# Optimization experiments

Measured on AMD Instinct MI355X. Metric: run time of the kernel, lower is better.

The kernel has to match this reference:

```python
import jax, jax.numpy as jnp
import numpy as np

EPS = 1e-8
LRELU_SLOPE = 0.2


def leaky_relu(x, p=LRELU_SLOPE):
    return jnp.where(x >= 0, x, p * x)


def conv2dmod(x, weight, style):
    """StyleGAN2 weight-demodulated conv.
    x: [B,C_in,H,W], weight: [C_out,C_in,k,k], style: [B,C_in]."""
    # per-sample modulation: scale input channels by (style + 1)
    w = weight[None] * (style[:, None, :, None, None] + 1.0)  # [B,O,I,k,k]
    # demodulation: rescale each output filter to unit norm
    d = jax.lax.rsqrt(jnp.sum(w * w, axis=(2, 3, 4), keepdims=True) + EPS)
    w = w * d

    def conv_one(xi, wi):
        # xi: [C_in,H,W], wi: [O,I,k,k] -> [O,H,W]
        return jax.lax.conv_general_dilated(
            xi[None], wi, window_strides=(1, 1), padding='SAME',
            dimension_numbers=('NCHW', 'OIHW', 'NCHW'))[0]

    return jax.vmap(conv_one)(x, w)  # [B,O,H,W]


def setup_inputs() -> dict:
    key = jax.random.key(0)
    ks = jax.random.split(key, 9)
    B, C_in, C_out, H, W = 16, 128, 256, 128, 128
    return {
        "features": jax.random.normal(ks[0], (B, C_in, H, W), jnp.float32),
        "style_mean1": jax.random.normal(ks[1], (B, C_in, 1, 1), jnp.float32),
        "style_std1": jax.random.normal(ks[2], (B, C_in, 1, 1), jnp.float32),
        "style_mean2": jax.random.normal(ks[3], (B, C_in, 1, 1), jnp.float32),
        "style_std2": jax.random.normal(ks[4], (B, C_in, 1, 1), jnp.float32),
        "lastBlockBool": 0,
        "w1": jax.random.normal(ks[5], (C_in, C_in, 3, 3), jnp.float32),
        "w2": jax.random.normal(ks[6], (C_in, C_in, 3, 3), jnp.float32),
        "down_w": jax.random.normal(ks[7], (C_out, C_in, 4, 4), jnp.float32) * 0.05,
        "down_b": jnp.zeros((C_out,), jnp.float32),
    }


def reference(features, style_mean1, style_std1, style_mean2, style_std2,
              lastBlockBool, w1, w2, down_w, down_b):
    # style_mean2/style_std2/lastBlockBool are accepted but unused by the
    # original forward; dropout is identity (eval mode).
    s1 = style_mean1[:, :, 0, 0]  # squeeze(-1).squeeze(-1) -> [B,C_in]
    s2 = style_std1[:, :, 0, 0]
    x = leaky_relu(conv2dmod(features, w1, s1))
    x = leaky_relu(conv2dmod(x, w2, s2) + x)  # residual
    # downsample: 4x4 conv, stride 2, pad 1 -> halves H,W
    y = jax.lax.conv_general_dilated(
        x, down_w, window_strides=(2, 2), padding=((1, 1), (1, 1)),
        dimension_numbers=('NCHW', 'OIHW', 'NCHW'))
    return y + down_b[None, :, None, None]
```

## Files before the change

kernel.cpp:

```cpp
#include <hip/hip_runtime.h>
#include <hip/hip_bf16.h>

constexpr int B  = 16;
constexpr int C  = 128;
constexpr int H  = 128;
constexpr int W  = 128;
constexpr int CO = 256;
constexpr int HO = 64;
constexpr int WO = 64;

#define EPSV   1e-8f
#define SLOPE  0.2f

typedef short bf16x8 __attribute__((ext_vector_type(8)));
typedef float f32x4  __attribute__((ext_vector_type(4)));

typedef const __attribute__((address_space(1))) unsigned int  gbl_u32;
typedef __attribute__((address_space(3))) unsigned int        lds_u32;

__device__ __forceinline__ void bar_raw() {
    asm volatile("" ::: "memory");
    __builtin_amdgcn_s_barrier();
    asm volatile("" ::: "memory");
}
#define WAITV(N) asm volatile("s_waitcnt vmcnt(" #N ")" ::: "memory")

__device__ __forceinline__ short f2bs(float v) {
    __hip_bfloat16 h = __float2bfloat16(v);
    return *(short*)&h;
}
__device__ __forceinline__ float bs2f(short s) {
    __hip_bfloat16 h = *(__hip_bfloat16*)&s;
    return __bfloat162float(h);
}

__global__ __launch_bounds__(128) void demod_kernel(
    const float* __restrict__ w1, const float* __restrict__ w2,
    const float* __restrict__ s1, const float* __restrict__ s2,
    float* __restrict__ d)
{
    int bid  = blockIdx.x;
    int conv = bid >> 11;
    int b    = (bid >> 7) & 15;
    int o    = bid & 127;
    const float* w = conv ? w2 : w1;
    const float* s = conv ? s2 : s1;
    int i = threadIdx.x;
    float sv = s[b * C + i] + 1.0f;
    const float* wp = w + (o * C + i) * 9;
    float sum = 0.f;
    #pragma unroll
    for (int k = 0; k < 9; ++k) { float t = wp[k] * sv; sum += t * t; }
    #pragma unroll
    for (int off = 32; off; off >>= 1) sum += __shfl_down(sum, off);
    __shared__ float red[2];
    if ((threadIdx.x & 63) == 0) red[threadIdx.x >> 6] = sum;
    __syncthreads();
    if (threadIdx.x == 0) d[bid] = rsqrtf(red[0] + red[1] + EPSV);
}

__global__ __launch_bounds__(256) void expand_kernel(
    const float* __restrict__ w1, const float* __restrict__ w2,
    const float* __restrict__ s1, const float* __restrict__ s2,
    const float* __restrict__ d, short* __restrict__ wm)
{
    int idx = blockIdx.x * 256 + threadIdx.x;
    int ic  = idx & 127;
    int oc  = (idx >> 7) & 127;
    int t   = idx >> 14;
    int tap = t % 9;
    int cb  = t / 9;
    int b   = cb & 15;
    int conv= cb >> 4;
    const float* w = conv ? w2 : w1;
    const float* s = conv ? s2 : s1;
    float v = w[(oc * C + ic) * 9 + tap] * (s[b * C + ic] + 1.0f)
            * d[(conv * B + b) * C + oc];
    int icH = ic >> 6, icL = (ic >> 5) & 1;
    int dst = cb * 147456
            + ((icH * 18 + tap * 2 + icL) * 8 + (oc >> 4)) * 512
            + ((ic >> 3) & 3) * 128 + (oc & 15) * 8 + (ic & 7);
    wm[dst] = f2bs(v);
}

__global__ __launch_bounds__(256) void dwexpand_kernel(
    const float* __restrict__ dw, short* __restrict__ dwm)
{
    int idx = blockIdx.x * 256 + threadIdx.x;
    int ic  = idx & 127;
    int oc  = (idx >> 7) & 255;
    int tap = idx >> 15;
    int dst = ((ic >> 5) * 16 + tap) * 8192 + (oc >> 7) * 4096
            + ((oc >> 4) & 7) * 512
            + ((ic >> 3) & 3) * 128 + (oc & 15) * 8 + (ic & 7);
    dwm[dst] = f2bs(dw[(oc * C + ic) * 16 + tap]);
}

__global__ __launch_bounds__(256) void nchw2nhwc_kernel(
    const float* __restrict__ in, short* __restrict__ out)
{
    __shared__ short s[128 * 136];
    int bid = blockIdx.x;
    int h = bid & 127, b = bid >> 7;
    int tid = threadIdx.x;
    for (int i = tid; i < 128 * 32; i += 256) {
        int w4 = i & 31, ic = i >> 5;
        float4 v = *(const float4*)&in[((b * C + ic) * H + h) * W + w4 * 4];
        s[(w4 * 4 + 0) * 136 + ic] = f2bs(v.x);
        s[(w4 * 4 + 1) * 136 + ic] = f2bs(v.y);
        s[(w4 * 4 + 2) * 136 + ic] = f2bs(v.z);
        s[(w4 * 4 + 3) * 136 + ic] = f2bs(v.w);
    }
    __syncthreads();
    for (int i = tid; i < 128 * 16; i += 256) {
        int icg = i & 15, w = i >> 4;
        *(uint4*)&out[((b * H + h) * W + w) * C + icg * 8] =
            *(uint4*)&s[w * 136 + icg * 8];
    }
}

__global__ __launch_bounds__(256, 4) void conv3x3_mfma(
    const short* __restrict__ in, const short* __restrict__ wmc,
    const short* __restrict__ res, short* __restrict__ out)
{
    __shared__ short sIn[180 * 64];
    __shared__ short sW[2][4096];

    int bid = blockIdx.x;
    int wt = bid & 7, ht = (bid >> 3) & 15, b = bid >> 7;
    int w0 = wt * 16, h0 = ht * 8;
    int tid  = threadIdx.x;
    int lane = tid & 63, wv = tid >> 6;
    int q = lane >> 4, l15 = lane & 15;
    int wr = wv & 1;
    int wc = wv >> 1;

    const short* wb = wmc + b * 147456;

    auto stageIn = [&](int st) {
        for (int i = tid; i < 180 * 8; i += 256) {
            int slot = i & 7, pix = i >> 3;
            int hl = pix / 18, wl = pix - hl * 18;
            int gh = h0 - 1 + hl, gw = w0 - 1 + wl;
            uint4 v = make_uint4(0u, 0u, 0u, 0u);
            if ((unsigned)gh < (unsigned)H && (unsigned)gw < (unsigned)W)
                v = *(const uint4*)&in[((b * H + gh) * W + gw) * C + st * 64 + slot * 8];
            *(uint4*)&sIn[pix * 64 + ((slot ^ (pix & 7)) << 3)] = v;
        }
    };
    auto stageW = [&](int st, int s, int buf) {
        #pragma unroll
        for (int i = 0; i < 2; ++i) {
            const short* g = wb + st * 73728 + s * 4096
                           + (wv * 2 + i) * 512 + lane * 8;
            __builtin_amdgcn_global_load_lds(
                (gbl_u32*)g, (lds_u32*)&sW[buf][(wv * 2 + i) * 512], 16, 0, 0);
        }
    };

    f32x4 acc[4][4];
    #pragma unroll
    for (int mt = 0; mt < 4; ++mt)
        #pragma unroll
        for (int nt = 0; nt < 4; ++nt)
            acc[mt][nt] = (f32x4){0.f, 0.f, 0.f, 0.f};

    stageW(0, 0, 0);
    stageIn(0);
    __syncthreads();

    int bfbase = q * 128 + l15 * 8;

    #pragma unroll 1
    for (int st = 0; st < 2; ++st) {
        #pragma unroll 2
        for (int s = 0; s < 18; ++s) {
            int tap = s >> 1, icL = s & 1;
            int dh = tap / 3, dwd = tap - dh * 3;
            if (s < 17)        stageW(st, s + 1, (s + 1) & 1);
            else if (st == 0)  stageW(1, 0, 0);
            if (st == 1 && s == 17) { WAITV(0); } else { WAITV(2); }
            bar_raw();
            bf16x8 af[4], bf[4];
            #pragma unroll
            for (int mt = 0; mt < 4; ++mt) {
                int pix  = (wr * 4 + mt + dh) * 18 + l15 + dwd;
                int slot = (icL * 4 + q) ^ (pix & 7);
                af[mt] = *(const bf16x8*)&sIn[pix * 64 + slot * 8];
            }
            #pragma unroll
            for (int nt = 0; nt < 4; ++nt)
                bf[nt] = *(const bf16x8*)&sW[s & 1][(wc * 4 + nt) * 512 + bfbase];
            #pragma unroll
            for (int mt = 0; mt < 4; ++mt)
                #pragma unroll
                for (int nt = 0; nt < 4; ++nt)
                    acc[mt][nt] = __builtin_amdgcn_mfma_f32_16x16x32_bf16(
                        af[mt], bf[nt], acc[mt][nt], 0, 0, 0);
            bar_raw();
        }
        if (st == 0) { stageIn(1); __syncthreads(); }
    }

    bool has_res = (res != nullptr);
    #pragma unroll
    for (int mt = 0; mt < 4; ++mt) {
        int h = h0 + wr * 4 + mt;
        #pragma unroll
        for (int nt = 0; nt < 4; ++nt) {
            int oc = wc * 64 + nt * 16 + l15;
            #pragma unroll
            for (int reg = 0; reg < 4; ++reg) {
                int w = w0 + q * 4 + reg;
                int idx = ((b * H + h) * W + w) * C + oc;
                float v = acc[mt][nt][reg];
                if (has_res) v += bs2f(res[idx]);
                v = v >= 0.f ? v : SLOPE * v;
                out[idx] = f2bs(v);
            }
        }
    }
}

__global__ __launch_bounds__(256, 2) void downconv_mfma(
    const short* __restrict__ in, const short* __restrict__ dwm,
    const float* __restrict__ db, float* __restrict__ out)
{
    __shared__ short sIn[2 * 306 * 32];
    __shared__ short sW[2][4096];

    int bid = blockIdx.x;
    int wt = bid & 3;
    int ht = (bid >> 2) & 7;
    int ot = (bid >> 5) & 1;
    int b  = bid >> 6;
    int ow0 = wt * 16, oh0 = ht * 8, oc0 = ot * 128;
    int ih0 = 2 * oh0 - 1, iw0 = 2 * ow0 - 1;

    int tid  = threadIdx.x;
    int lane = tid & 63, wv = tid >> 6;
    int q = lane >> 4, l15 = lane & 15;

    const short* wbase = dwm + ot * 4096;

    auto stageIn = [&](int icC) {
        for (int i = tid; i < 612 * 4; i += 256) {
            int slot = i & 3, pix = i >> 2;
            int ihl = pix / 34, iwl = pix - ihl * 34;
            int gh = ih0 + ihl, gw = iw0 + iwl;
            uint4 v = make_uint4(0u, 0u, 0u, 0u);
            if ((unsigned)gh < (unsigned)H && (unsigned)gw < (unsigned)W)
                v = *(const uint4*)&in[((b * H + gh) * W + gw) * C + icC * 32 + slot * 8];
            int par = iwl & 1, pl = ihl * 17 + (iwl >> 1);
            *(uint4*)&sIn[(par * 306 + pl) * 32 + ((slot ^ ((pl >> 1) & 3)) << 3)] = v;
        }
    };
    auto stageW = [&](int step, int buf) {
        #pragma unroll
        for (int j = 0; j < 2; ++j) {
            int base = (wv * 2 + j) * 512;
            const short* g = wbase + step * 8192 + base + lane * 8;
            __builtin_amdgcn_global_load_lds(
                (gbl_u32*)g, (lds_u32*)&sW[buf][base], 16, 0, 0);
        }
    };

    f32x4 acc[2][8];
    #pragma unroll
    for (int mt = 0; mt < 2; ++mt)
        #pragma unroll
        for (int nt = 0; nt < 8; ++nt)
            acc[mt][nt] = (f32x4){0.f, 0.f, 0.f, 0.f};

    stageW(0, 0);
    stageIn(0);
    __syncthreads();

    int afbase = q * 128 + l15 * 8;

    #pragma unroll 1
    for (int icC = 0; icC < 4; ++icC) {
        #pragma unroll 2
        for (int tap = 0; tap < 16; ++tap) {
            int step = icC * 16 + tap;
            if (step < 63) stageW(step + 1, (step + 1) & 1);
            if (step < 63) { WAITV(2); } else { WAITV(0); }
            bar_raw();
            int dh = tap >> 2, dwn = tap & 3;
            int par = dwn & 1, cb0 = dwn >> 1;
            bf16x8 af[2], bf[8];
            #pragma unroll
            for (int mt = 0; mt < 2; ++mt)
                af[mt] = *(const bf16x8*)&sW[step & 1][(wv * 2 + mt) * 512 + afbase];
            #pragma unroll
            for (int nt = 0; nt < 8; ++nt) {
                int pl = (2 * nt + dh) * 17 + cb0 + l15;
                bf[nt] = *(const bf16x8*)&sIn[(par * 306 + pl) * 32
                                              + ((q ^ ((pl >> 1) & 3)) << 3)];
            }
            #pragma unroll
            for (int mt = 0; mt < 2; ++mt)
                #pragma unroll
                for (int nt = 0; nt < 8; ++nt)
                    acc[mt][nt] = __builtin_amdgcn_mfma_f32_16x16x32_bf16(
                        af[mt], bf[nt], acc[mt][nt], 0, 0, 0);
            bar_raw();
        }
        if (icC < 3) { stageIn(icC + 1); __syncthreads(); }
    }

    #pragma unroll
    for (int mt = 0; mt < 2; ++mt) {
        f32x4 bi = *(const f32x4*)&db[oc0 + (wv * 2 + mt) * 16 + q * 4];
        #pragma unroll
        for (int nt = 0; nt < 8; ++nt) {
            int oh = oh0 + nt;
            #pragma unroll
            for (int reg = 0; reg < 4; ++reg) {
                int oc = oc0 + (wv * 2 + mt) * 16 + q * 4 + reg;
                out[((b * CO + oc) * HO + oh) * WO + ow0 + l15] =
                    acc[mt][nt][reg] + bi[reg];
            }
        }
    }
}

extern "C" void kernel_launch(void* const* d_in, const int* in_sizes, int n_in,
                              void* d_out, int out_size, void* d_ws, size_t ws_size,
                              hipStream_t stream) {
    const float* features = (const float*)d_in[0];
    const float* sm1      = (const float*)d_in[1];
    const float* ss1      = (const float*)d_in[2];
    const float* w1       = (const float*)d_in[6];
    const float* w2       = (const float*)d_in[7];
    const float* dw       = (const float*)d_in[8];
    const float* db       = (const float*)d_in[9];
    float* out = (float*)d_out;

    char* ws = (char*)d_ws;
    short* x1  = (short*)ws;
    short* x2  = (short*)(ws + 67108864);
    short* wm  = (short*)(ws + 134217728);
    short* dwm = (short*)(ws + 143654912);
    float* dv  = (float*)(ws + 144703488);

    demod_kernel    <<<4096, 128, 0, stream>>>(w1, w2, sm1, ss1, dv);
    expand_kernel   <<<18432, 256, 0, stream>>>(w1, w2, sm1, ss1, dv, wm);
    dwexpand_kernel <<<2048, 256, 0, stream>>>(dw, dwm);
    nchw2nhwc_kernel<<<2048, 256, 0, stream>>>(features, x2);
    conv3x3_mfma    <<<2048, 256, 0, stream>>>(x2, wm, nullptr, x1);
    conv3x3_mfma    <<<2048, 256, 0, stream>>>(x1, wm + 16 * 147456, x1, x2);
    downconv_mfma   <<<1024, 256, 0, stream>>>(x2, dwm, db, out);
}
```

Measured before the change: 327.0 us.

## Triple-buffer weight tiles with one barrier per step and padded LDS layout

In both MFMA conv kernels the weight ring buffer grows from two to three slots, prefetching two steps ahead. This removes the trailing barrier of each step, so there is one barrier per iteration instead of two. The XOR-swizzled input layout in shared memory is replaced by padded rows (72 and 40 shorts), which makes the address arithmetic simpler and the loops fully unrolled. The cost is more shared memory, a lower occupancy hint for conv3x3 (launch bounds 4 to 3), larger code, and a possible change in bank-conflict behaviour.

```diff
diff --git a/kernel.cpp b/kernel.cpp
--- a/kernel.cpp
+++ b/kernel.cpp
@@ -119,12 +119,12 @@
     }
 }
 
-__global__ __launch_bounds__(256, 4) void conv3x3_mfma(
+__global__ __launch_bounds__(256, 3) void conv3x3_mfma(
     const short* __restrict__ in, const short* __restrict__ wmc,
     const short* __restrict__ res, short* __restrict__ out)
 {
-    __shared__ short sIn[180 * 64];
-    __shared__ short sW[2][4096];
+    __shared__ short sW[3][4096];
+    __shared__ short sIn[180 * 72];
 
     int bid = blockIdx.x;
     int wt = bid & 7, ht = (bid >> 3) & 15, b = bid >> 7;
@@ -145,16 +145,16 @@
             uint4 v = make_uint4(0u, 0u, 0u, 0u);
             if ((unsigned)gh < (unsigned)H && (unsigned)gw < (unsigned)W)
                 v = *(const uint4*)&in[((b * H + gh) * W + gw) * C + st * 64 + slot * 8];
-            *(uint4*)&sIn[pix * 64 + ((slot ^ (pix & 7)) << 3)] = v;
+            *(uint4*)&sIn[pix * 72 + slot * 8] = v;
         }
     };
-    auto stageW = [&](int st, int s, int buf) {
+    auto stageW = [&](int s) {
         #pragma unroll
         for (int i = 0; i < 2; ++i) {
-            const short* g = wb + st * 73728 + s * 4096
+            const short* g = wb + (s / 18) * 73728 + (s % 18) * 4096
                            + (wv * 2 + i) * 512 + lane * 8;
             __builtin_amdgcn_global_load_lds(
-                (gbl_u32*)g, (lds_u32*)&sW[buf][(wv * 2 + i) * 512], 16, 0, 0);
+                (gbl_u32*)g, (lds_u32*)&sW[s % 3][(wv * 2 + i) * 512], 16, 0, 0);
         }
     };
 
@@ -165,41 +165,39 @@
         for (int nt = 0; nt < 4; ++nt)
             acc[mt][nt] = (f32x4){0.f, 0.f, 0.f, 0.f};
 
-    stageW(0, 0, 0);
-    stageIn(0);
+    stageW(0); stageW(1); stageIn(0);
     __syncthreads();
 
-    int bfbase = q * 128 + l15 * 8;
-
-    #pragma unroll 1
-    for (int st = 0; st < 2; ++st) {
-        #pragma unroll 2
-        for (int s = 0; s < 18; ++s) {
-            int tap = s >> 1, icL = s & 1;
-            int dh = tap / 3, dwd = tap - dh * 3;
-            if (s < 17)        stageW(st, s + 1, (s + 1) & 1);
-            else if (st == 0)  stageW(1, 0, 0);
-            if (st == 1 && s == 17) { WAITV(0); } else { WAITV(2); }
+    const int abase = ((wr * 4) * 18 + l15) * 72 + q * 8;
+    const int bbase = q * 128 + l15 * 8;
+
+    #pragma unroll
+    for (int s = 0; s < 36; ++s) {
+        if (s == 18) {
             bar_raw();
-            bf16x8 af[4], bf[4];
-            #pragma unroll
-            for (int mt = 0; mt < 4; ++mt) {
-                int pix  = (wr * 4 + mt + dh) * 18 + l15 + dwd;
-                int slot = (icL * 4 + q) ^ (pix & 7);
-                af[mt] = *(const bf16x8*)&sIn[pix * 64 + slot * 8];
-            }
+            stageIn(1);
+            __syncthreads();
+        } else {
+            if (s == 35) { WAITV(0); } else { WAITV(2); }
+            bar_raw();
+        }
+        if (s + 2 < 36) stageW(s + 2);
+        const int loc = s % 18, tap = loc >> 1, icL = loc & 1;
+        const int dh = tap / 3, dwd = tap - dh * 3;
+        bf16x8 af[4], bf[4];
+        #pragma unroll
+        for (int mt = 0; mt < 4; ++mt)
+            af[mt] = *(const bf16x8*)&sIn[abase + ((mt + dh) * 18 + dwd) * 72
+                                          + icL * 32];
+        #pragma unroll
+        for (int nt = 0; nt < 4; ++nt)
+            bf[nt] = *(const bf16x8*)&sW[s % 3][(wc * 4 + nt) * 512 + bbase];
+        #pragma unroll
+        for (int mt = 0; mt < 4; ++mt)
             #pragma unroll
             for (int nt = 0; nt < 4; ++nt)
-                bf[nt] = *(const bf16x8*)&sW[s & 1][(wc * 4 + nt) * 512 + bfbase];
-            #pragma unroll
-            for (int mt = 0; mt < 4; ++mt)
-                #pragma unroll
-                for (int nt = 0; nt < 4; ++nt)
-                    acc[mt][nt] = __builtin_amdgcn_mfma_f32_16x16x32_bf16(
-                        af[mt], bf[nt], acc[mt][nt], 0, 0, 0);
-            bar_raw();
-        }
-        if (st == 0) { stageIn(1); __syncthreads(); }
+                acc[mt][nt] = __builtin_amdgcn_mfma_f32_16x16x32_bf16(
+                    af[mt], bf[nt], acc[mt][nt], 0, 0, 0);
     }
 
     bool has_res = (res != nullptr);
@@ -226,8 +224,8 @@
     const short* __restrict__ in, const short* __restrict__ dwm,
     const float* __restrict__ db, float* __restrict__ out)
 {
-    __shared__ short sIn[2 * 306 * 32];
-    __shared__ short sW[2][4096];
+    __shared__ short sW[3][4096];
+    __shared__ short sIn[612 * 40];
 
     int bid = blockIdx.x;
     int wt = bid & 3;
@@ -251,17 +249,16 @@
             uint4 v = make_uint4(0u, 0u, 0u, 0u);
             if ((unsigned)gh < (unsigned)H && (unsigned)gw < (unsigned)W)
                 v = *(const uint4*)&in[((b * H + gh) * W + gw) * C + icC * 32 + slot * 8];
-            int par = iwl & 1, pl = ihl * 17 + (iwl >> 1);
-            *(uint4*)&sIn[(par * 306 + pl) * 32 + ((slot ^ ((pl >> 1) & 3)) << 3)] = v;
+            int row = (iwl & 1) * 306 + ihl * 17 + (iwl >> 1);
+            *(uint4*)&sIn[row * 40 + slot * 8] = v;
         }
     };
-    auto stageW = [&](int step, int buf) {
+    auto stageW = [&](int s) {
         #pragma unroll
         for (int j = 0; j < 2; ++j) {
-            int base = (wv * 2 + j) * 512;
-            const short* g = wbase + step * 8192 + base + lane * 8;
+            const short* g = wbase + s * 8192 + (wv * 2 + j) * 512 + lane * 8;
             __builtin_amdgcn_global_load_lds(
-                (gbl_u32*)g, (lds_u32*)&sW[buf][base], 16, 0, 0);
+                (gbl_u32*)g, (lds_u32*)&sW[s % 3][(wv * 2 + j) * 512], 16, 0, 0);
         }
     };
 
@@ -272,41 +269,40 @@
         for (int nt = 0; nt < 8; ++nt)
             acc[mt][nt] = (f32x4){0.f, 0.f, 0.f, 0.f};
 
-    stageW(0, 0);
-    stageIn(0);
+    stageW(0); stageW(1); stageIn(0);
     __syncthreads();
 
-    int afbase = q * 128 + l15 * 8;
-
-    #pragma unroll 1
-    for (int icC = 0; icC < 4; ++icC) {
-        #pragma unroll 2
-        for (int tap = 0; tap < 16; ++tap) {
-            int step = icC * 16 + tap;
-            if (step < 63) stageW(step + 1, (step + 1) & 1);
-            if (step < 63) { WAITV(2); } else { WAITV(0); }
+    const int abase = q * 128 + l15 * 8;
+    const int pbase = l15 * 40 + q * 8;
+
+    #pragma unroll
+    for (int s = 0; s < 64; ++s) {
+        if (s > 0 && (s & 15) == 0) {
             bar_raw();
-            int dh = tap >> 2, dwn = tap & 3;
-            int par = dwn & 1, cb0 = dwn >> 1;
-            bf16x8 af[2], bf[8];
+            stageIn(s >> 4);
+            __syncthreads();
+        } else {
+            if (s == 63) { WAITV(0); } else { WAITV(2); }
+            bar_raw();
+        }
+        if (s + 2 < 64) stageW(s + 2);
+        const int tap = s & 15;
+        const int dh = tap >> 2, dwn = tap & 3;
+        const int par = dwn & 1, cb0 = dwn >> 1;
+        bf16x8 af[2], bf[8];
+        #pragma unroll
+        for (int mt = 0; mt < 2; ++mt)
+            af[mt] = *(const bf16x8*)&sW[s % 3][(wv * 2 + mt) * 512 + abase];
+        #pragma unroll
+        for (int nt = 0; nt < 8; ++nt)
+            bf[nt] = *(const bf16x8*)&sIn[(par * 306 + (2 * nt + dh) * 17 + cb0) * 40
+                                          + pbase];
+        #pragma unroll
+        for (int mt = 0; mt < 2; ++mt)
             #pragma unroll
-            for (int mt = 0; mt < 2; ++mt)
-                af[mt] = *(const bf16x8*)&sW[step & 1][(wv * 2 + mt) * 512 + afbase];
-            #pragma unroll
-            for (int nt = 0; nt < 8; ++nt) {
-                int pl = (2 * nt + dh) * 17 + cb0 + l15;
-                bf[nt] = *(const bf16x8*)&sIn[(par * 306 + pl) * 32
-                                              + ((q ^ ((pl >> 1) & 3)) << 3)];
-            }
-            #pragma unroll
-            for (int mt = 0; mt < 2; ++mt)
-                #pragma unroll
-                for (int nt = 0; nt < 8; ++nt)
-                    acc[mt][nt] = __builtin_amdgcn_mfma_f32_16x16x32_bf16(
-                        af[mt], bf[nt], acc[mt][nt], 0, 0, 0);
-            bar_raw();
-        }
-        if (icC < 3) { stageIn(icC + 1); __syncthreads(); }
+            for (int nt = 0; nt < 8; ++nt)
+                acc[mt][nt] = __builtin_amdgcn_mfma_f32_16x16x32_bf16(
+                    af[mt], bf[nt], acc[mt][nt], 0, 0, 0);
     }
 
     #pragma unroll
```

Result: slower. 342.7 us (+4.8%).
